# Kernel optimization log

Hardware: AMD Instinct MI355X
Metric: run time of the kernel (lower is better)

The kernel has to match this reference:

```python
import jax, jax.numpy as jnp
import numpy as np


def setup_inputs() -> dict:
    key = jax.random.key(0)
    kq, kk, kv = jax.random.split(key, 3)
    B, H, N, D = 2, 16, 2048, 128
    q = jax.random.normal(kq, (B, H, N, D), dtype=jnp.float32)
    k = jax.random.normal(kk, (B, H, N, D), dtype=jnp.float32)
    v = jax.random.normal(kv, (B, H, N, D), dtype=jnp.float32)
    return {"q": q, "k": k, "v": v, "num_sink": 4, "window_size": 1024}


def reference(q, k, v, num_sink, window_size):
    # Sink + sliding-window causal attention (single-device path of the SP wrapper).
    # Query i attends to key j iff j <= i AND (j < num_sink OR i - j < window_size).
    B, H, N, D = q.shape
    scale = 1.0 / np.sqrt(D).astype(np.float32)
    i = jnp.arange(N)[:, None]   # query positions
    j = jnp.arange(N)[None, :]   # key positions
    mask = (j <= i) & ((j < num_sink) | ((i - j) < window_size))  # [N, N]
    scores = jnp.einsum('bhid,bhjd->bhij', q, k) * scale          # [B,H,N,N]
    scores = jnp.where(mask, scores, jnp.finfo(scores.dtype).min)
    attn = jax.nn.softmax(scores, axis=-1)
    return jnp.einsum('bhij,bhjd->bhid', attn, v)
```

## Files before the change

### kernel.cpp

```cpp
#include <hip/hip_runtime.h>
#include <stdint.h>

#define NN 2048
#define DD 128
#define BHH 32
#define QT 64
#define KT 64

typedef short v8s __attribute__((ext_vector_type(8)));
typedef float v4f __attribute__((ext_vector_type(4)));

__device__ __forceinline__ unsigned short f2bf(float x) {
  unsigned u = __builtin_bit_cast(unsigned, x);
  u += 0x7fffu + ((u >> 16) & 1u);
  return (unsigned short)(u >> 16);
}

__device__ __forceinline__ v8s cvt8(const float* __restrict__ p) {
  v8s r;
#pragma unroll
  for (int j = 0; j < 8; j++) r[j] = (short)f2bf(p[j]);
  return r;
}

__global__ void kconv(const float* __restrict__ src, unsigned short* __restrict__ dst) {
  size_t i = ((size_t)blockIdx.x * 256 + threadIdx.x) * 8;
  *(v8s*)(dst + i) = cvt8(src + i);
}

__global__ void vtranspose(const float* __restrict__ V, unsigned short* __restrict__ Vt) {
  __shared__ unsigned short t[32][33];
  int bh = blockIdx.z;
  int n0 = blockIdx.x * 32, d0 = blockIdx.y * 32;
  int x = threadIdx.x, y = threadIdx.y;
  const float* src = V + ((size_t)bh * NN + n0) * DD + d0;
#pragma unroll
  for (int i = y; i < 32; i += 8) t[i][x] = f2bf(src[(size_t)i * DD + x]);
  __syncthreads();
  unsigned short* dst = Vt + ((size_t)bh * DD + d0) * NN + n0;
#pragma unroll
  for (int i = y; i < 32; i += 8) dst[(size_t)i * NN + x] = t[x][i];
}

template <bool KBF, bool USE_VT>
__global__ __launch_bounds__(256, 4) void attn(
    const float* __restrict__ Q,
    const float* __restrict__ Kf, const unsigned short* __restrict__ Kb,
    const unsigned short* __restrict__ Vt, const float* __restrict__ Vf,
    const int* __restrict__ nsp, const int* __restrict__ wsp,
    float* __restrict__ O) {
  const int ns = nsp[0], win = wsp[0];
  const int bh = blockIdx.y;
  const int q0 = blockIdx.x * QT;
  const int tid = threadIdx.x;
  const int w = tid >> 6;
  const int l = tid & 63;
  const int lo = l & 15, q4 = l >> 4;

  __shared__ __align__(16) unsigned short Kl[KT * DD];
  __shared__ __align__(16) unsigned short Vl[KT * DD];
  __shared__ __align__(16) unsigned short Pl[4 * 16 * KT];

  v8s qf[4];
  {
    const float* qb = Q + ((size_t)bh * NN + q0 + w * 16 + lo) * DD + q4 * 8;
#pragma unroll
    for (int kc = 0; kc < 4; kc++) qf[kc] = cvt8(qb + kc * 32);
  }

  float lsum[4];
  v4f oa[8];
#pragma unroll
  for (int r = 0; r < 4; r++) lsum[r] = 0.f;
#pragma unroll
  for (int nc = 0; nc < 8; nc++) oa[nc] = (v4f){0.f, 0.f, 0.f, 0.f};

  const float csc = 0.088388347648318447f * 1.4426950408889634f;

  const size_t koff0 = ((size_t)bh * NN + w * 16 + lo) * DD + q4 * 8;
  unsigned short* Pw = Pl + w * 1024;
  const int qrow0 = q0 + w * 16;
  const int rb = q4 * 4;

  for (int kb = 0; kb < q0 + QT; kb += KT) {
    if ((kb >= ns) && (kb + KT - 1 < q0 - win + 1)) continue;

    v8s kst[4];
    {
      size_t g = koff0 + (size_t)kb * DD;
#pragma unroll
      for (int kc = 0; kc < 4; kc++)
        kst[kc] = KBF ? *(const v8s*)(Kb + g + kc * 32) : cvt8(Kf + g + kc * 32);
    }
    v8s vst[4];
    if (USE_VT) {
#pragma unroll
      for (int i = 0; i < 4; i++) {
        int f = w * 4 + i, kt = f >> 3, nc = f & 7;
        vst[i] = *(const v8s*)(Vt + ((size_t)bh * DD + nc * 16 + lo) * NN + kb +
                               kt * 32 + q4 * 8);
      }
    }

    __syncthreads();
#pragma unroll
    for (int kc = 0; kc < 4; kc++)
      *(v8s*)(Kl + (w * 4 + kc) * 512 + l * 8) = kst[kc];
    if (USE_VT) {
#pragma unroll
      for (int i = 0; i < 4; i++)
        *(v8s*)(Vl + (w * 4 + i) * 512 + l * 8) = vst[i];
    }
    __syncthreads();

    v4f s[4];
#pragma unroll
    for (int ct = 0; ct < 4; ct++) {
      s[ct] = (v4f){0.f, 0.f, 0.f, 0.f};
#pragma unroll
      for (int kc = 0; kc < 4; kc++) {
        v8s kf = *(const v8s*)(Kl + (ct * 4 + kc) * 512 + l * 8);
        s[ct] = __builtin_amdgcn_mfma_f32_16x16x32_bf16(qf[kc], kf, s[ct], 0, 0, 0);
      }
    }
#pragma unroll
    for (int ct = 0; ct < 4; ct++) {
      int kj = kb + ct * 16 + lo;
#pragma unroll
      for (int r = 0; r < 4; r++) {
        int qi = qrow0 + rb + r;
        bool valid = (kj <= qi) && ((kj < ns) || (qi - kj < win));
        float e = valid ? __builtin_amdgcn_exp2f(s[ct][r] * csc) : 0.f;
        s[ct][r] = e;
      }
    }
#pragma unroll
    for (int r = 0; r < 4; r++)
      lsum[r] += (s[0][r] + s[1][r]) + (s[2][r] + s[3][r]);

#pragma unroll
    for (int ct = 0; ct < 4; ct++) {
#pragma unroll
      for (int r = 0; r < 4; r++) {
        int row = rb + r;
        int idx = (ct >> 1) * 512 + (row + 16 * ((ct & 1) * 2 + ((l >> 3) & 1))) * 8 + (l & 7);
        Pw[idx] = f2bf(s[ct][r]);
      }
    }
#pragma unroll
    for (int kt = 0; kt < 2; kt++) {
      v8s pf = *(const v8s*)(Pw + kt * 512 + l * 8);
#pragma unroll
      for (int nc = 0; nc < 8; nc++) {
        v8s vf;
        if (USE_VT) {
          vf = *(const v8s*)(Vl + (kt * 8 + nc) * 512 + l * 8);
        } else {
#pragma unroll
          for (int j = 0; j < 8; j++) {
            size_t vi = ((size_t)bh * NN + kb + kt * 32 + q4 * 8 + j) * DD + nc * 16 + lo;
            vf[j] = (short)f2bf(Vf[vi]);
          }
        }
        oa[nc] = __builtin_amdgcn_mfma_f32_16x16x32_bf16(pf, vf, oa[nc], 0, 0, 0);
      }
    }
  }

  float inv[4];
#pragma unroll
  for (int r = 0; r < 4; r++) {
    float v = lsum[r];
    v += __shfl_xor(v, 1, 64);
    v += __shfl_xor(v, 2, 64);
    v += __shfl_xor(v, 4, 64);
    v += __shfl_xor(v, 8, 64);
    inv[r] = 1.f / v;
  }
  float* ob = O + ((size_t)bh * NN + qrow0) * DD;
#pragma unroll
  for (int nc = 0; nc < 8; nc++)
#pragma unroll
    for (int r = 0; r < 4; r++)
      ob[(size_t)(rb + r) * DD + nc * 16 + lo] = oa[nc][r] * inv[r];
}

extern "C" void kernel_launch(void* const* d_in, const int* in_sizes, int n_in,
                              void* d_out, int out_size, void* d_ws, size_t ws_size,
                              hipStream_t stream) {
  const float* q = (const float*)d_in[0];
  const float* k = (const float*)d_in[1];
  const float* v = (const float*)d_in[2];
  const int* nsp = (const int*)d_in[3];
  const int* wsp = (const int*)d_in[4];
  float* out = (float*)d_out;

  const size_t half = (size_t)BHH * NN * DD * sizeof(unsigned short);
  unsigned short* kbf = (unsigned short*)d_ws;
  unsigned short* vt = (unsigned short*)((char*)d_ws + half);

  if (ws_size >= 2 * half) {
    kconv<<<(BHH * NN * DD / 8 + 255) / 256, 256, 0, stream>>>(k, kbf);
    vtranspose<<<dim3(NN / 32, DD / 32, BHH), dim3(32, 8), 0, stream>>>(v, vt);
    attn<true, true><<<dim3(NN / QT, BHH), 256, 0, stream>>>(q, k, kbf, vt, v, nsp, wsp, out);
  } else if (ws_size >= half) {
    vtranspose<<<dim3(NN / 32, DD / 32, BHH), dim3(32, 8), 0, stream>>>(v, (unsigned short*)d_ws);
    attn<false, true><<<dim3(NN / QT, BHH), 256, 0, stream>>>(q, k, nullptr, (unsigned short*)d_ws, v, nsp, wsp, out);
  } else {
    attn<false, false><<<dim3(NN / QT, BHH), 256, 0, stream>>>(q, k, nullptr, nullptr, v, nsp, wsp, out);
  }
}
```

Measured before the change: 220.8 us.

## Drop K pre-conversion, vectorize V transpose, schedule heaviest query tiles first

Removes the separate K fp32-to-bf16 conversion kernel, so the attention kernel converts K on the fly from fp32 loads. The V transpose now uses 64x64 tiles with vectorized float4 loads and 8-wide bf16 stores. The grid is reordered with batch-head on x and reversed query tiles, so the longest causal tiles launch first and blocks for the same query tile run together. The trade-off is one fewer kernel launch and less intermediate traffic, against K being read as fp32 and converted again by every query tile that reuses it.

```diff
diff --git a/kernel.cpp b/kernel.cpp
--- a/kernel.cpp
+++ b/kernel.cpp
@@ -8,6 +8,7 @@
 #define KT 64
 
 typedef short v8s __attribute__((ext_vector_type(8)));
+typedef short v4s __attribute__((ext_vector_type(4)));
 typedef float v4f __attribute__((ext_vector_type(4)));
 
 __device__ __forceinline__ unsigned short f2bf(float x) {
@@ -23,35 +24,44 @@
   return r;
 }
 
-__global__ void kconv(const float* __restrict__ src, unsigned short* __restrict__ dst) {
-  size_t i = ((size_t)blockIdx.x * 256 + threadIdx.x) * 8;
-  *(v8s*)(dst + i) = cvt8(src + i);
-}
-
 __global__ void vtranspose(const float* __restrict__ V, unsigned short* __restrict__ Vt) {
-  __shared__ unsigned short t[32][33];
-  int bh = blockIdx.z;
-  int n0 = blockIdx.x * 32, d0 = blockIdx.y * 32;
-  int x = threadIdx.x, y = threadIdx.y;
+  __shared__ unsigned short t[64 * 68];
+  const int bh = blockIdx.z;
+  const int n0 = blockIdx.x * 64, d0 = blockIdx.y * 64;
+  const int tid = threadIdx.x;
   const float* src = V + ((size_t)bh * NN + n0) * DD + d0;
 #pragma unroll
-  for (int i = y; i < 32; i += 8) t[i][x] = f2bf(src[(size_t)i * DD + x]);
+  for (int p = 0; p < 4; p++) {
+    int r = p * 16 + (tid >> 4);
+    int c = (tid & 15) * 4;
+    v4f f = *(const v4f*)(src + (size_t)r * DD + c);
+    v4s u;
+#pragma unroll
+    for (int j = 0; j < 4; j++) u[j] = (short)f2bf(f[j]);
+    *(v4s*)(t + r * 68 + c) = u;
+  }
   __syncthreads();
   unsigned short* dst = Vt + ((size_t)bh * DD + d0) * NN + n0;
 #pragma unroll
-  for (int i = y; i < 32; i += 8) dst[(size_t)i * NN + x] = t[x][i];
-}
-
-template <bool KBF, bool USE_VT>
+  for (int p = 0; p < 2; p++) {
+    int d = p * 32 + (tid >> 3);
+    int nc = (tid & 7) * 8;
+    v8s o;
+#pragma unroll
+    for (int j = 0; j < 8; j++) o[j] = (short)t[(nc + j) * 68 + d];
+    *(v8s*)(dst + (size_t)d * NN + nc) = o;
+  }
+}
+
+template <bool USE_VT>
 __global__ __launch_bounds__(256, 4) void attn(
-    const float* __restrict__ Q,
-    const float* __restrict__ Kf, const unsigned short* __restrict__ Kb,
+    const float* __restrict__ Q, const float* __restrict__ Kf,
     const unsigned short* __restrict__ Vt, const float* __restrict__ Vf,
     const int* __restrict__ nsp, const int* __restrict__ wsp,
     float* __restrict__ O) {
   const int ns = nsp[0], win = wsp[0];
-  const int bh = blockIdx.y;
-  const int q0 = blockIdx.x * QT;
+  const int bh = blockIdx.x;
+  const int q0 = (gridDim.y - 1 - blockIdx.y) * QT;
   const int tid = threadIdx.x;
   const int w = tid >> 6;
   const int l = tid & 63;
@@ -87,10 +97,9 @@
 
     v8s kst[4];
     {
-      size_t g = koff0 + (size_t)kb * DD;
-#pragma unroll
-      for (int kc = 0; kc < 4; kc++)
-        kst[kc] = KBF ? *(const v8s*)(Kb + g + kc * 32) : cvt8(Kf + g + kc * 32);
+      const float* g = Kf + koff0 + (size_t)kb * DD;
+#pragma unroll
+      for (int kc = 0; kc < 4; kc++) kst[kc] = cvt8(g + kc * 32);
     }
     v8s vst[4];
     if (USE_VT) {
@@ -130,8 +139,7 @@
       for (int r = 0; r < 4; r++) {
         int qi = qrow0 + rb + r;
         bool valid = (kj <= qi) && ((kj < ns) || (qi - kj < win));
-        float e = valid ? __builtin_amdgcn_exp2f(s[ct][r] * csc) : 0.f;
-        s[ct][r] = e;
+        s[ct][r] = valid ? __builtin_amdgcn_exp2f(s[ct][r] * csc) : 0.f;
       }
     }
 #pragma unroll
@@ -195,18 +203,12 @@
   const int* wsp = (const int*)d_in[4];
   float* out = (float*)d_out;
 
-  const size_t half = (size_t)BHH * NN * DD * sizeof(unsigned short);
-  unsigned short* kbf = (unsigned short*)d_ws;
-  unsigned short* vt = (unsigned short*)((char*)d_ws + half);
-
-  if (ws_size >= 2 * half) {
-    kconv<<<(BHH * NN * DD / 8 + 255) / 256, 256, 0, stream>>>(k, kbf);
-    vtranspose<<<dim3(NN / 32, DD / 32, BHH), dim3(32, 8), 0, stream>>>(v, vt);
-    attn<true, true><<<dim3(NN / QT, BHH), 256, 0, stream>>>(q, k, kbf, vt, v, nsp, wsp, out);
-  } else if (ws_size >= half) {
-    vtranspose<<<dim3(NN / 32, DD / 32, BHH), dim3(32, 8), 0, stream>>>(v, (unsigned short*)d_ws);
-    attn<false, true><<<dim3(NN / QT, BHH), 256, 0, stream>>>(q, k, nullptr, (unsigned short*)d_ws, v, nsp, wsp, out);
+  const size_t vt_bytes = (size_t)BHH * NN * DD * sizeof(unsigned short);
+  if (ws_size >= vt_bytes) {
+    unsigned short* vt = (unsigned short*)d_ws;
+    vtranspose<<<dim3(NN / 64, DD / 64, BHH), 256, 0, stream>>>(v, vt);
+    attn<true><<<dim3(BHH, NN / QT), 256, 0, stream>>>(q, k, vt, v, nsp, wsp, out);
   } else {
-    attn<false, false><<<dim3(NN / QT, BHH), 256, 0, stream>>>(q, k, nullptr, nullptr, v, nsp, wsp, out);
-  }
-}
+    attn<false><<<dim3(BHH, NN / QT), 256, 0, stream>>>(q, k, nullptr, v, nsp, wsp, out);
+  }
+}
```

Measured after the change: 226.6 us. 2.6% more time.
